# Kernel optimization log

Measured on AMD Instinct MI355X. Metric: run time of the kernel, lower is better.

The kernel has to match this reference:

```python
import jax, jax.numpy as jnp
import numpy as np

B, T, C, H = 8, 2048, 768, 12
D = C // H

def setup_inputs() -> dict:
    key = jax.random.key(0)
    ks = jax.random.split(key, 5)
    s = 0.02
    return {
        "x": jax.random.normal(ks[0], (B, T, C), dtype=jnp.float32),
        "w_attn": jax.random.normal(ks[1], (C, 3 * C), dtype=jnp.float32) * s,
        "b_attn": jnp.zeros((3 * C,), dtype=jnp.float32),
        "w_proj": jax.random.normal(ks[2], (C, C), dtype=jnp.float32) * s,
        "b_proj": jnp.zeros((C,), dtype=jnp.float32),
    }

def reference(x, w_attn, b_attn, w_proj, b_proj):
    Bx, Tx, Cx = x.shape
    qkv = x @ w_attn + b_attn                       # [B,T,3C]
    q, k, v = jnp.split(qkv, 3, axis=-1)
    # [B,H,T,D]
    q = q.reshape(Bx, Tx, H, D).transpose(0, 2, 1, 3)
    k = k.reshape(Bx, Tx, H, D).transpose(0, 2, 1, 3)
    v = v.reshape(Bx, Tx, H, D).transpose(0, 2, 1, 3)
    scale = 1.0 / jnp.sqrt(jnp.float32(D))
    att = jnp.einsum('bhqd,bhkd->bhqk', q, k) * scale
    causal = jnp.tril(jnp.ones((Tx, Tx), dtype=bool))
    att = jnp.where(causal[None, None], att, -jnp.inf)
    att = jax.nn.softmax(att, axis=-1)
    y = jnp.einsum('bhqk,bhkd->bhqd', att, v)
    y = y.transpose(0, 2, 1, 3).reshape(Bx, Tx, Cx)
    y = y @ w_proj + b_proj
    return y, k, v
```

## Files before the change

kernel.cpp:

```cpp
#include <hip/hip_runtime.h>
#include <hip/hip_bf16.h>
#include <stdint.h>

#define Bz 8
#define Tz 2048
#define Cz 768
#define Hz 12
#define Dz 64
#define Mz (Bz*Tz)
#define N3 (3*Cz)
#define YSZ ((size_t)Mz*Cz)

#define SCL 0.18033688011112042f
#define KVB 64
#define QBLK 128

typedef __bf16 bf16;
typedef __attribute__((ext_vector_type(8))) bf16 bf16x8;
typedef __attribute__((ext_vector_type(4))) bf16 bf16x4;
typedef __attribute__((ext_vector_type(4))) float f32x4;

#define MFMA(A_,B_,C_) __builtin_amdgcn_mfma_f32_16x16x32_bf16(A_,B_,C_,0,0,0)

__device__ __forceinline__ void gll16(const void* g, void* l) {
  __builtin_amdgcn_global_load_lds(
      (const __attribute__((address_space(1))) void*)g,
      (__attribute__((address_space(3))) void*)l, 16, 0, 0);
}

__global__ __launch_bounds__(256) void prep_x(const float* __restrict__ x,
                                              bf16* __restrict__ xb) {
  int i = blockIdx.x*blockDim.x + threadIdx.x;
  int stride = gridDim.x*blockDim.x;
  const float4* x4 = (const float4*)x;
  int n4 = (int)(YSZ/4);
  for (int j = i; j < n4; j += stride) {
    float4 f = x4[j];
    bf16x4 o = { (bf16)f.x, (bf16)f.y, (bf16)f.z, (bf16)f.w };
    *(bf16x4*)(xb + 4*(size_t)j) = o;
  }
}

__global__ __launch_bounds__(256) void transpose_conv(const float* __restrict__ src,
                                                      bf16* __restrict__ dst,
                                                      int R, int Ncol) {
  __shared__ float tile[32][33];
  int bx = blockIdx.x, by = blockIdx.y;
  int tx = threadIdx.x & 31, ty = threadIdx.x >> 5;
  #pragma unroll
  for (int i = 0; i < 4; ++i)
    tile[ty + 8*i][tx] = src[(size_t)(by*32 + ty + 8*i)*Ncol + bx*32 + tx];
  __syncthreads();
  #pragma unroll
  for (int i = 0; i < 4; ++i)
    dst[(size_t)(bx*32 + ty + 8*i)*R + by*32 + tx] = (bf16)tile[tx][ty + 8*i];
}

template<int EPI>
__global__ __launch_bounds__(256) void gemm128(
    const bf16* __restrict__ A, const bf16* __restrict__ Bt,
    int Kdim, int Mtiles, int Ntiles,
    const float* __restrict__ bias,
    bf16* __restrict__ qws, bf16* __restrict__ kws, bf16* __restrict__ vtb,
    float* __restrict__ kout, float* __restrict__ vout,
    float* __restrict__ yout)
{
  __shared__ alignas(16) bf16 sA[128*64];
  __shared__ alignas(16) bf16 sB[128*64];
  int nwg = Mtiles*Ntiles;
  int bid = blockIdx.x;
  int cpx = nwg >> 3;
  int swz = (bid & 7)*cpx + (bid >> 3);
  int mtile = swz % Mtiles, ntile = swz / Mtiles;
  int tid = threadIdx.x, w = tid >> 6, l = tid & 63;
  int wr = w >> 1, wc = w & 1;
  const int rowBase = mtile*128, colBase = ntile*128;

  f32x4 acc[4][4] = {};

  int rbase = tid >> 3;
  int ch    = tid & 7;
  int swk   = (ch ^ (rbase & 7)) << 3;
  const bf16* gA = A + (size_t)(rowBase + rbase)*Kdim + swk;
  const bf16* gB = Bt + (size_t)(colBase + rbase)*Kdim + swk;
  char* lA = (char*)sA + w*1024;
  char* lB = (char*)sB + w*1024;

  int lr = l & 15, lg = l >> 4;

  for (int k0 = 0; k0 < Kdim; k0 += 64) {
    #pragma unroll
    for (int p = 0; p < 4; ++p) {
      gll16(gA + (size_t)(p*32)*Kdim, lA + p*4096);
      gll16(gB + (size_t)(p*32)*Kdim, lB + p*4096);
    }
    gA += 64; gB += 64;
    __syncthreads();
    #pragma unroll
    for (int kk = 0; kk < 2; ++kk) {
      bf16x8 af[4], bfr[4];
      int cc = ((kk*4 + lg) ^ (lr & 7)) << 4;
      #pragma unroll
      for (int m = 0; m < 4; ++m)
        af[m] = *(const bf16x8*)((const char*)sA + (wr*64 + m*16 + lr)*128 + cc);
      #pragma unroll
      for (int n = 0; n < 4; ++n)
        bfr[n] = *(const bf16x8*)((const char*)sB + (wc*64 + n*16 + lr)*128 + cc);
      #pragma unroll
      for (int m = 0; m < 4; ++m)
        #pragma unroll
        for (int n = 0; n < 4; ++n)
          acc[m][n] = MFMA(af[m], bfr[n], acc[m][n]);
    }
    __syncthreads();
  }

  #pragma unroll
  for (int m = 0; m < 4; ++m) {
    #pragma unroll
    for (int n = 0; n < 4; ++n) {
      int gcol = colBase + wc*64 + n*16 + lr;
      float bv = bias[gcol];
      int grow0 = rowBase + wr*64 + m*16 + lg*4;
      if (EPI == 1) {
        #pragma unroll
        for (int r = 0; r < 4; ++r)
          yout[(size_t)(grow0 + r)*Cz + gcol] = acc[m][n][r] + bv;
      } else {
        int which = gcol / Cz;
        int within = gcol - which*Cz;
        int h = within >> 6, d = within & 63;
        int bidx = grow0 >> 11;
        int t0 = grow0 & 2047;
        size_t bhTD = ((size_t)bidx*Hz + h);
        if (which == 0) {
          bf16* qp = qws + (bhTD*Tz + t0)*Dz + d;
          #pragma unroll
          for (int r = 0; r < 4; ++r)
            qp[(size_t)r*Dz] = (bf16)((acc[m][n][r] + bv) * SCL);
        } else if (which == 1) {
          float* kp = kout + (bhTD*Tz + t0)*Dz + d;
          bf16*  kp2 = kws + (bhTD*Tz + t0)*Dz + d;
          #pragma unroll
          for (int r = 0; r < 4; ++r) {
            float v = acc[m][n][r] + bv;
            kp[(size_t)r*Dz] = v;
            kp2[(size_t)r*Dz] = (bf16)v;
          }
        } else {
          float* vp = vout + (bhTD*Tz + t0)*Dz + d;
          bf16x4 pk;
          #pragma unroll
          for (int r = 0; r < 4; ++r) {
            float v = acc[m][n][r] + bv;
            vp[(size_t)r*Dz] = v;
            pk[r] = (bf16)v;
          }
          int ts = (t0 & ~31) | (((t0 >> 2) & 3) << 3) | (((t0 >> 4) & 1) << 2) | (t0 & 3);
          *(bf16x4*)(vtb + (bhTD*Dz + d)*Tz + ts) = pk;
        }
      }
    }
  }
}

__device__ __forceinline__ void stageKV(const bf16* kgb, const bf16* vgb, int kv0,
                                        char* cK, char* cV, int tid, int w) {
  int off = tid*16;
  int row = off >> 7, ch = (off >> 4) & 7;
  int sw = ((ch ^ (row & 7)) << 3);
  gll16(kgb + (size_t)(kv0 + row)*Dz + sw, cK + w*1024);
  gll16(vgb + (size_t)row*Tz + kv0 + sw,   cV + w*1024);
}

__device__ __forceinline__ void attn_tile(
    int kv0, int qminw, int qmaxw, int q_l, int lr, int lg,
    const char* cK, const char* cV,
    const bf16x8& qf0, const bf16x8& qf1,
    f32x4 (&o)[4], float& mrun, float& lrun)
{
  const f32x4 zf = {0.f, 0.f, 0.f, 0.f};
  f32x4 s[4];
  __builtin_amdgcn_s_setprio(1);
  #pragma unroll
  for (int n = 0; n < 4; ++n) {
    int kvb = kv0 + n*16;
    if (kvb <= qmaxw) {
      int row = n*16 + lr;
      int c0 = lg ^ (lr & 7);
      bf16x8 kf0 = *(const bf16x8*)(cK + row*128 + (c0 << 4));
      bf16x8 kf1 = *(const bf16x8*)(cK + row*128 + ((c0 ^ 4) << 4));
      f32x4 t = MFMA(kf0, qf0, zf);
      s[n] = MFMA(kf1, qf1, t);
    } else {
      s[n][0] = -1e30f; s[n][1] = -1e30f; s[n][2] = -1e30f; s[n][3] = -1e30f;
    }
  }
  __builtin_amdgcn_s_setprio(0);
  #pragma unroll
  for (int n = 0; n < 4; ++n) {
    int kvb = kv0 + n*16;
    if (kvb <= qmaxw && kvb + 15 > qminw) {
      #pragma unroll
      for (int r = 0; r < 4; ++r)
        s[n][r] = (kvb + 4*lg + r <= q_l) ? s[n][r] : -1e30f;
    }
  }
  f32x4 a0;
  #pragma unroll
  for (int r = 0; r < 4; ++r)
    a0[r] = fmaxf(fmaxf(s[0][r], s[1][r]), fmaxf(s[2][r], s[3][r]));
  float mx = fmaxf(fmaxf(a0[0], a0[1]), fmaxf(a0[2], a0[3]));
  mx = fmaxf(mx, __shfl_xor(mx, 16));
  mx = fmaxf(mx, __shfl_xor(mx, 32));

  bool skip = __all(mx <= mrun + 8.0f);
  float corr = 1.0f;
  if (!skip) {
    float mnew = fmaxf(mrun, mx);
    corr = exp2f(mrun - mnew);
    mrun = mnew;
  }
  f32x4 acc4 = zf;
  #pragma unroll
  for (int n = 0; n < 4; ++n) {
    #pragma unroll
    for (int r = 0; r < 4; ++r) {
      float e = exp2f(s[n][r] - mrun);
      s[n][r] = e;
      acc4[r] += e;
    }
  }
  float rs = (acc4[0] + acc4[1]) + (acc4[2] + acc4[3]);
  rs += __shfl_xor(rs, 16);
  rs += __shfl_xor(rs, 32);
  if (!skip) {
    lrun = lrun*corr + rs;
    float c0_ = __shfl(corr, 4*lg + 0);
    float c1_ = __shfl(corr, 4*lg + 1);
    float c2_ = __shfl(corr, 4*lg + 2);
    float c3_ = __shfl(corr, 4*lg + 3);
    #pragma unroll
    for (int nd = 0; nd < 4; ++nd) {
      o[nd][0] *= c0_; o[nd][1] *= c1_; o[nd][2] *= c2_; o[nd][3] *= c3_;
    }
  } else {
    lrun += rs;
  }
  __builtin_amdgcn_s_setprio(1);
  #pragma unroll
  for (int kk = 0; kk < 2; ++kk) {
    if (kv0 + kk*32 <= qmaxw) {
      bf16x8 pf;
      pf[0] = (bf16)s[2*kk][0];   pf[1] = (bf16)s[2*kk][1];
      pf[2] = (bf16)s[2*kk][2];   pf[3] = (bf16)s[2*kk][3];
      pf[4] = (bf16)s[2*kk+1][0]; pf[5] = (bf16)s[2*kk+1][1];
      pf[6] = (bf16)s[2*kk+1][2]; pf[7] = (bf16)s[2*kk+1][3];
      int cb = (kk*4 + lg) ^ (lr & 7);
      #pragma unroll
      for (int nd = 0; nd < 4; ++nd) {
        bf16x8 vf = *(const bf16x8*)(cV + (nd*16 + lr)*128 + (cb << 4));
        o[nd] = MFMA(pf, vf, o[nd]);
      }
    }
  }
  __builtin_amdgcn_s_setprio(0);
}

__global__ __launch_bounds__(512, 6) void attn128(
    const bf16* __restrict__ qws, const bf16* __restrict__ kb,
    const bf16* __restrict__ vtb, bf16* __restrict__ yatt)
{
  __shared__ alignas(16) char sK[2][8192];
  __shared__ alignas(16) char sV[2][8192];
  int bid = blockIdx.x;
  int qb = (Tz/QBLK) - 1 - bid/(Bz*Hz);
  int bh = bid % (Bz*Hz);
  int b = bh / Hz, h = bh - b*Hz;
  int tid = threadIdx.x, w = tid >> 6, l = tid & 63;
  int lr = l & 15, lg = l >> 4;
  const int q0 = qb*QBLK;
  const int qminw = q0 + w*16;
  const int qmaxw = qminw + 15;
  const int q_l = qminw + lr;

  const bf16* qbase = qws + ((size_t)bh*Tz + qminw + lr)*Dz + lg*8;
  bf16x8 qf0 = *(const bf16x8*)qbase;
  bf16x8 qf1 = *(const bf16x8*)(qbase + 32);

  f32x4 o[4] = {};
  float mrun = -1e30f, lrun = 0.f;

  const bf16* kgb = kb  + (size_t)bh*Tz*Dz;
  const bf16* vgb = vtb + (size_t)bh*Dz*Tz;

  int nT = 2*qb + 2;
  stageKV(kgb, vgb, 0, sK[0], sV[0], tid, w);
  int buf = 0;
  for (int kt = 0; kt + 1 < nT; ++kt) {
    stageKV(kgb, vgb, (kt + 1)*KVB, sK[buf ^ 1], sV[buf ^ 1], tid, w);
    asm volatile("s_waitcnt vmcnt(2)" ::: "memory");
    __builtin_amdgcn_s_barrier();
    __builtin_amdgcn_sched_barrier(0);
    attn_tile(kt*KVB, qminw, qmaxw, q_l, lr, lg, sK[buf], sV[buf],
              qf0, qf1, o, mrun, lrun);
    asm volatile("s_waitcnt lgkmcnt(0)" ::: "memory");
    __builtin_amdgcn_s_barrier();
    __builtin_amdgcn_sched_barrier(0);
    buf ^= 1;
  }
  asm volatile("s_waitcnt vmcnt(0)" ::: "memory");
  __builtin_amdgcn_s_barrier();
  __builtin_amdgcn_sched_barrier(0);
  attn_tile((nT - 1)*KVB, qminw, qmaxw, q_l, lr, lg, sK[buf], sV[buf],
            qf0, qf1, o, mrun, lrun);

  float inv = 1.0f / lrun;
  float i0 = __shfl(inv, 4*lg + 0);
  float i1 = __shfl(inv, 4*lg + 1);
  float i2 = __shfl(inv, 4*lg + 2);
  float i3 = __shfl(inv, 4*lg + 3);
  #pragma unroll
  for (int nd = 0; nd < 4; ++nd) {
    int d = nd*16 + lr;
    int t0 = q0 + w*16 + lg*4;
    bf16* yp = yatt + ((size_t)(b*Tz + t0))*Cz + h*Dz + d;
    yp[0*Cz]   = (bf16)(o[nd][0] * i0);
    yp[1*Cz]   = (bf16)(o[nd][1] * i1);
    yp[2*Cz]   = (bf16)(o[nd][2] * i2);
    yp[3*Cz]   = (bf16)(o[nd][3] * i3);
  }
}

extern "C" void kernel_launch(void* const* d_in, const int* in_sizes, int n_in,
                              void* d_out, int out_size, void* d_ws, size_t ws_size,
                              hipStream_t stream) {
  const float* x      = (const float*)d_in[0];
  const float* w_attn = (const float*)d_in[1];
  const float* b_attn = (const float*)d_in[2];
  const float* w_proj = (const float*)d_in[3];
  const float* b_proj = (const float*)d_in[4];

  float* y    = (float*)d_out;
  float* kout = y + YSZ;
  float* vout = y + 2*YSZ;

  char* ws = (char*)d_ws;
  bf16* xb   = (bf16*)ws;
  bf16* qws  = (bf16*)(ws + 25165824);
  bf16* kb   = (bf16*)(ws + 50331648);
  bf16* vtb  = (bf16*)(ws + 75497472);
  bf16* wtA  = (bf16*)(ws + 100663296);
  bf16* wtP  = (bf16*)(ws + 104202240);
  bf16* yatt = xb;

  prep_x<<<2048, 256, 0, stream>>>(x, xb);
  transpose_conv<<<dim3(N3/32, Cz/32), 256, 0, stream>>>(w_attn, wtA, Cz, N3);
  transpose_conv<<<dim3(Cz/32, Cz/32), 256, 0, stream>>>(w_proj, wtP, Cz, Cz);

  gemm128<0><<<dim3((Mz/128)*(N3/128)), 256, 0, stream>>>(
      xb, wtA, Cz, Mz/128, N3/128, b_attn, qws, kb, vtb, kout, vout, nullptr);

  attn128<<<dim3((Tz/QBLK)*(Bz*Hz)), 512, 0, stream>>>(qws, kb, vtb, yatt);

  gemm128<1><<<dim3((Mz/128)*(Cz/128)), 256, 0, stream>>>(
      yatt, wtP, Cz, Mz/128, Cz/128, b_proj, nullptr, nullptr, nullptr,
      nullptr, nullptr, y);
}
```

Baseline: 303.1 us.

## Double-buffer GEMM LDS tiles with async prefetch and explicit waitcnt barriers

Turns the GEMM k-loop into a two-stage pipeline. While MFMAs run on the current LDS buffer, direct global-to-LDS loads fill the other buffer, using vmcnt waits and raw s_barrier calls instead of __syncthreads. It also raises wave priority around the MFMA block and changes the tile swizzle so N varies fastest instead of M. LDS use doubles to 64KB per block, which may lower occupancy.

```diff
diff --git a/kernel.cpp b/kernel.cpp
--- a/kernel.cpp
+++ b/kernel.cpp
@@ -65,13 +65,13 @@
     float* __restrict__ kout, float* __restrict__ vout,
     float* __restrict__ yout)
 {
-  __shared__ alignas(16) bf16 sA[128*64];
-  __shared__ alignas(16) bf16 sB[128*64];
+  __shared__ alignas(16) bf16 sA[2][128*64];
+  __shared__ alignas(16) bf16 sB[2][128*64];
   int nwg = Mtiles*Ntiles;
   int bid = blockIdx.x;
   int cpx = nwg >> 3;
   int swz = (bid & 7)*cpx + (bid >> 3);
-  int mtile = swz % Mtiles, ntile = swz / Mtiles;
+  int ntile = swz % Ntiles, mtile = swz / Ntiles;
   int tid = threadIdx.x, w = tid >> 6, l = tid & 63;
   int wr = w >> 1, wc = w & 1;
   const int rowBase = mtile*128, colBase = ntile*128;
@@ -83,36 +83,61 @@
   int swk   = (ch ^ (rbase & 7)) << 3;
   const bf16* gA = A + (size_t)(rowBase + rbase)*Kdim + swk;
   const bf16* gB = Bt + (size_t)(colBase + rbase)*Kdim + swk;
-  char* lA = (char*)sA + w*1024;
-  char* lB = (char*)sB + w*1024;
 
   int lr = l & 15, lg = l >> 4;
-
-  for (int k0 = 0; k0 < Kdim; k0 += 64) {
+  int nK = Kdim >> 6;
+
+  {
+    char* lA = (char*)sA[0] + w*1024;
+    char* lB = (char*)sB[0] + w*1024;
     #pragma unroll
     for (int p = 0; p < 4; ++p) {
       gll16(gA + (size_t)(p*32)*Kdim, lA + p*4096);
       gll16(gB + (size_t)(p*32)*Kdim, lB + p*4096);
     }
     gA += 64; gB += 64;
-    __syncthreads();
+  }
+  int buf = 0;
+  for (int t = 0; t < nK; ++t) {
+    if (t + 1 < nK) {
+      char* lA = (char*)sA[buf ^ 1] + w*1024;
+      char* lB = (char*)sB[buf ^ 1] + w*1024;
+      #pragma unroll
+      for (int p = 0; p < 4; ++p) {
+        gll16(gA + (size_t)(p*32)*Kdim, lA + p*4096);
+        gll16(gB + (size_t)(p*32)*Kdim, lB + p*4096);
+      }
+      gA += 64; gB += 64;
+      asm volatile("s_waitcnt vmcnt(8)" ::: "memory");
+    } else {
+      asm volatile("s_waitcnt vmcnt(0)" ::: "memory");
+    }
+    __builtin_amdgcn_s_barrier();
+    __builtin_amdgcn_sched_barrier(0);
+    const char* cA = (const char*)sA[buf];
+    const char* cB = (const char*)sB[buf];
+    __builtin_amdgcn_s_setprio(1);
     #pragma unroll
     for (int kk = 0; kk < 2; ++kk) {
       bf16x8 af[4], bfr[4];
       int cc = ((kk*4 + lg) ^ (lr & 7)) << 4;
       #pragma unroll
       for (int m = 0; m < 4; ++m)
-        af[m] = *(const bf16x8*)((const char*)sA + (wr*64 + m*16 + lr)*128 + cc);
+        af[m] = *(const bf16x8*)(cA + (wr*64 + m*16 + lr)*128 + cc);
       #pragma unroll
       for (int n = 0; n < 4; ++n)
-        bfr[n] = *(const bf16x8*)((const char*)sB + (wc*64 + n*16 + lr)*128 + cc);
+        bfr[n] = *(const bf16x8*)(cB + (wc*64 + n*16 + lr)*128 + cc);
       #pragma unroll
       for (int m = 0; m < 4; ++m)
         #pragma unroll
         for (int n = 0; n < 4; ++n)
           acc[m][n] = MFMA(af[m], bfr[n], acc[m][n]);
     }
-    __syncthreads();
+    __builtin_amdgcn_s_setprio(0);
+    asm volatile("s_waitcnt lgkmcnt(0)" ::: "memory");
+    __builtin_amdgcn_s_barrier();
+    __builtin_amdgcn_sched_barrier(0);
+    buf ^= 1;
   }
 
   #pragma unroll
```

Result: faster. 261.5 us (-13.7%).
